# Optimization experiments

Hardware: AMD Instinct MI355X
Metric: run time of the kernel (lower is better)

## Reference

```python
import jax, jax.numpy as jnp
import numpy as np

VOCAB_SIZE = 128
HIDDEN_DIM = 128
NUM_STATES = 64
STACK_VOCAB_SIZE = 32
STACK_DEPTH = 64
NUM_MEM_ACTIONS = 2 + STACK_VOCAB_SIZE  # 0=NOOP, 1=POP, k>=2 => PUSH symbol (k-2)
NUM_BUF_ACTIONS = VOCAB_SIZE
T, B = 512, 512


def setup_inputs() -> dict:
    key = jax.random.key(0)
    ks = jax.random.split(key, 10)
    return {
        "x": jax.random.randint(ks[0], (T, B), 0, VOCAB_SIZE),
        "true_act": jax.random.randint(ks[1], (T, B), 0, NUM_MEM_ACTIONS),
        "true_s": jax.random.randint(ks[2], (T, B), 0, NUM_STATES),
        "use_forcing": jax.random.randint(ks[3], (T, B), 0, 2),
        "embed": jax.random.normal(ks[4], (VOCAB_SIZE, HIDDEN_DIM), jnp.float32) * 0.02,
        "W_mem": jax.random.normal(ks[5], (HIDDEN_DIM + NUM_STATES + STACK_VOCAB_SIZE, NUM_MEM_ACTIONS), jnp.float32) * 0.05,
        "b_mem": jnp.zeros((NUM_MEM_ACTIONS,), jnp.float32),
        "W_buf": jax.random.normal(ks[6], (HIDDEN_DIM + NUM_STATES + STACK_VOCAB_SIZE, NUM_BUF_ACTIONS), jnp.float32) * 0.05,
        "b_buf": jnp.zeros((NUM_BUF_ACTIONS,), jnp.float32),
        "W_state": jax.random.normal(ks[7], (HIDDEN_DIM + NUM_STATES + STACK_VOCAB_SIZE, NUM_STATES), jnp.float32) * 0.05,
        "b_state": jnp.zeros((NUM_STATES,), jnp.float32),
    }


def update_stack(stack, ptr, action):
    # stack: [STACK_DEPTH] int, ptr: [] int, action: [] int
    is_push = action >= 2
    is_pop = action == 1
    new_ptr = jnp.clip(ptr + jnp.where(is_push, 1, 0) - jnp.where(is_pop, 1, 0), 0, STACK_DEPTH - 1)
    sym = jnp.maximum(action - 2, 0)
    stack_new = stack.at[new_ptr].set(jnp.where(is_push, sym, stack[new_ptr]))
    r_new = stack_new[new_ptr]  # read top of stack
    return stack_new, new_ptr, r_new


def reference(x, true_act, true_s, use_forcing, embed, W_mem, b_mem, W_buf, b_buf, W_state, b_state):
    def step(carry, inp):
        stack, ptr, r_prev, s_prev = carry
        x_t, t_act, t_s, forcing = inp
        x_emb = embed[x_t]                                   # [B, H] gather
        s_emb = jax.nn.one_hot(s_prev, NUM_STATES, dtype=embed.dtype)
        r_emb = jax.nn.one_hot(r_prev, STACK_VOCAB_SIZE, dtype=embed.dtype)
        flat = jnp.concatenate([x_emb, s_emb, r_emb], axis=-1)  # [B, 224]
        logits_mem = flat @ W_mem + b_mem
        logits_buf = flat @ W_buf + b_buf
        logits_state = flat @ W_state + b_state
        pred_act = jnp.argmax(logits_mem, axis=-1)
        pred_state = jnp.argmax(logits_state, axis=-1)
        action = jnp.where(forcing > 0, t_act, pred_act)
        next_s = jnp.where(forcing > 0, t_s, pred_state)
        stack_new, ptr_new, r_new = jax.vmap(update_stack)(stack, ptr, action)
        return (stack_new, ptr_new, r_new, next_s), (logits_mem, logits_buf, logits_state)

    init = (
        jnp.zeros((B, STACK_DEPTH), jnp.int32),
        jnp.zeros((B,), jnp.int32),
        jnp.zeros((B,), jnp.int32),
        jnp.zeros((B,), jnp.int32),
    )
    _, (lm, lb, ls) = jax.lax.scan(step, init, (x, true_act, true_s, use_forcing))
    return lm, lb, ls
```

## Files before the change

### kernel.cpp

```cpp
#include <hip/hip_runtime.h>
#include <stdint.h>
#include <limits.h>


#define TT 512
#define BB 512
#define HH 128
#define NSs 64
#define NMm 34
#define NBb 128

typedef unsigned short u16;
typedef float f2 __attribute__((ext_vector_type(2)));

__global__ __launch_bounds__(256) void precompute_M(
    const float* __restrict__ embed,
    const float* __restrict__ Wm, const float* __restrict__ bm,
    const float* __restrict__ Wb, const float* __restrict__ bb,
    const float* __restrict__ Ws, const float* __restrict__ bs,
    float* __restrict__ Mm32, float* __restrict__ Ms32,
    float* __restrict__ Mb32, float* __restrict__ MmT,
    float* __restrict__ MsT) {
  __shared__ double e[HH];
  const int v = blockIdx.x;
  const int tid = threadIdx.x;
  if (tid < HH) e[tid] = (double)embed[v * HH + tid];
  __syncthreads();
  if (tid < NMm) {
    const int j = tid;
    double acc = 0.0;
    for (int h = 0; h < HH; ++h) acc += e[h] * (double)Wm[h * NMm + j];
    const float r = (float)(acc + (double)bm[j]);
    Mm32[v * NMm + j] = r;
    MmT[j * 128 + v] = r;
  } else if (tid < NMm + NSs) {
    const int j = tid - NMm;
    double acc = 0.0;
    for (int h = 0; h < HH; ++h) acc += e[h] * (double)Ws[h * NSs + j];
    const float r = (float)(acc + (double)bs[j]);
    Ms32[v * NSs + j] = r;
    MsT[j * 128 + v] = r;
  } else if (tid < NMm + NSs + NBb) {
    const int j = tid - NMm - NSs;
    double acc = 0.0;
    for (int h = 0; h < HH; ++h) acc += e[h] * (double)Wb[h * NBb + j];
    Mb32[v * NBb + j] = (float)(acc + (double)bb[j]);
  }
}

__global__ __launch_bounds__(128) void build_lut(
    const float* __restrict__ Wm, const float* __restrict__ Ws,
    const float* __restrict__ MmT, const float* __restrict__ MsT,
    u16* __restrict__ lut) {
  __shared__ float wms[NMm], wmr[NMm], wss[NSs], wsr[NSs];
  const int s = blockIdx.x >> 5;
  const int r = blockIdx.x & 31;
  const int tid = threadIdx.x;
  if (tid < NMm) {
    wms[tid] = Wm[(128 + s) * NMm + tid];
    wmr[tid] = Wm[(192 + r) * NMm + tid];
  }
  if (tid < NSs) {
    wss[tid] = Ws[(128 + s) * NSs + tid];
    wsr[tid] = Ws[(192 + r) * NSs + tid];
  }
  __syncthreads();

  const int v = tid;
  int bestm = INT_MIN, act = 0;
#pragma unroll
  for (int j = 0; j < NMm; ++j) {
    const double val = (double)MmT[j * 128 + v] + (double)wms[j] + (double)wmr[j];
    const int iv = (int)(val * 67108864.0);
    if (iv > bestm) { bestm = iv; act = j; }
  }
  int bests = INT_MIN, ns = 0;
#pragma unroll
  for (int j = 0; j < NSs; ++j) {
    const double val = (double)MsT[j * 128 + v] + (double)wss[j] + (double)wsr[j];
    const int iv = (int)(val * 67108864.0);
    if (iv > bests) { bests = iv; ns = j; }
  }
  lut[(unsigned)blockIdx.x * 128 + v] = (u16)(act | (ns << 6));
}

__global__ __launch_bounds__(512, 1) void sm_fused(
    const int* __restrict__ x, const int* __restrict__ tact,
    const int* __restrict__ tstate, const int* __restrict__ forc,
    const u16* __restrict__ lut,
    const float* __restrict__ Wm, const float* __restrict__ Wb,
    const float* __restrict__ Ws,
    const float* __restrict__ Mm32, const float* __restrict__ Ms32,
    const float* __restrict__ Mb32, float* __restrict__ out) {
  __shared__ unsigned sPk[2][TT];
  __shared__ volatile u16 trajL[2][TT];
  __shared__ volatile unsigned cnt[2];
  const int tid = threadIdx.x;
  const int base = blockIdx.x * 2;
  if (tid < 2) cnt[tid] = 0;
  for (int i = tid; i < 2 * TT; i += 512) {
    const int c = i >> 9, t = i & (TT - 1);
    const int g = t * BB + base + c;
    sPk[c][t] = (unsigned)x[g] | ((unsigned)tact[g] << 8) |
                ((unsigned)tstate[g] << 16) | ((unsigned)forc[g] << 24);
  }
  __syncthreads();

  const int lane = tid & 63;
  const int w = tid >> 6;

  if (w < 2) {
    __builtin_amdgcn_s_setprio(1);
    const int c = w;
    int stackv = 0;
    int ptr = 0, rr = 0, s = 0;
    unsigned p0 = sPk[c][0], p1 = sPk[c][1], p2 = sPk[c][2];

    for (int t = 0; t < TT; ++t) {
      const unsigned p3 = sPk[c][t + 3 < TT ? t + 3 : TT - 1];
      const unsigned pk_s = __builtin_amdgcn_readfirstlane(p0);

      if (lane == 0) trajL[c][t] = (u16)(s | (rr << 8));

      int act, ns;
      if (pk_s >> 24) {
        act = (int)((p0 >> 8) & 63u);
        ns = (int)((p0 >> 16) & 63u);
      } else {
        const int idx = s * 4096 + rr * 128 + (int)(p0 & 127u);
        const int lv = lut[idx];
        act = lv & 63;
        ns = (lv >> 6) & 63;
      }

      const bool ispush = act >= 2;
      int npn = ptr + (ispush ? 1 : 0) - (act == 1 ? 1 : 0);
      npn = npn < 0 ? 0 : (npn > 63 ? 63 : npn);
      if (ispush && lane == npn) stackv = act - 2;
      rr = __builtin_amdgcn_ds_bpermute(npn * 4, stackv);
      ptr = npn;
      s = ns;

      if ((t & 7) == 7) {
        __threadfence_block();
        if (lane == 0) cnt[c] = (unsigned)(t + 1);
      }
      p0 = p1; p1 = p2; p2 = p3;
    }
  } else {
    const int c = (w - 2) & 1;
    const int j = (w - 2) >> 1;
    const int b = base + c;
    float* outLM = out;
    float* outLB = out + (size_t)TT * BB * NMm;
    float* outLS = out + (size_t)TT * BB * (NMm + NBb);

    for (int t = j; t < TT; t += 3) {
      while (cnt[c] <= (unsigned)t) __builtin_amdgcn_s_sleep(4);
      const unsigned pk = sPk[c][t];
      const int xv = (int)(pk & 127u);
      const int pr = trajL[c][t];
      const int s = pr & 255;
      const int r = pr >> 8;
      const int rs = 128 + s, rr = 192 + r;
      const int row = t * BB + b;
      if (lane < NMm)
        __builtin_nontemporal_store(
            Mm32[xv * NMm + lane] + Wm[rs * NMm + lane] + Wm[rr * NMm + lane],
            &outLM[(size_t)row * NMm + lane]);
      __builtin_nontemporal_store(
          Ms32[xv * NSs + lane] + Ws[rs * NSs + lane] + Ws[rr * NSs + lane],
          &outLS[(size_t)row * NSs + lane]);
      const f2 mb  = *(const f2*)&Mb32[xv * NBb + 2 * lane];
      const f2 wbs = *(const f2*)&Wb[rs * NBb + 2 * lane];
      const f2 wbr = *(const f2*)&Wb[rr * NBb + 2 * lane];
      f2 o;
      o.x = mb.x + wbs.x + wbr.x;
      o.y = mb.y + wbs.y + wbr.y;
      __builtin_nontemporal_store(o, (f2*)&outLB[(size_t)row * NBb + 2 * lane]);
    }
  }
}

extern "C" void kernel_launch(void* const* d_in, const int* in_sizes, int n_in,
                              void* d_out, int out_size, void* d_ws, size_t ws_size,
                              hipStream_t stream) {
  if (ws_size < 690176) return;

  const int* x     = (const int*)d_in[0];
  const int* tactp = (const int*)d_in[1];
  const int* tstp  = (const int*)d_in[2];
  const int* forcp = (const int*)d_in[3];
  const float* embed = (const float*)d_in[4];
  const float* Wm = (const float*)d_in[5];
  const float* bm = (const float*)d_in[6];
  const float* Wb = (const float*)d_in[7];
  const float* bb = (const float*)d_in[8];
  const float* Ws = (const float*)d_in[9];
  const float* bs = (const float*)d_in[10];

  char* wsp = (char*)d_ws;
  float* Mm32 = (float*)(wsp);
  float* Ms32 = (float*)(wsp + 17408);
  float* Mb32 = (float*)(wsp + 50176);
  float* MmT  = (float*)(wsp + 115712);
  float* MsT  = (float*)(wsp + 133120);
  u16*   lut  = (u16*)(wsp + 165888);

  precompute_M<<<128, 256, 0, stream>>>(embed, Wm, bm, Wb, bb, Ws, bs,
                                        Mm32, Ms32, Mb32, MmT, MsT);
  build_lut<<<2048, 128, 0, stream>>>(Wm, Ws, MmT, MsT, lut);
  sm_fused<<<256, 512, 0, stream>>>(x, tactp, tstp, forcp, lut,
                                    Wm, Wb, Ws, Mm32, Ms32, Mb32,
                                    (float*)d_out);
}
```

Measured before the change: 156.0 us.

## Use one batch column per block with sentinel-based per-step producer/consumer sync

Each block now handles a single batch element instead of two: one wave runs the serial stack recurrence and seven waves write the logits. Blocks double to 512 so more CUs take part in the serial chain. The periodic shared counter with a fence every 8 steps is replaced by writing a sentinel into each trajectory slot and having consumers poll that slot. This lets consumers start each step as soon as it is ready, at the cost of more polling and relying on volatile ordering of 16-bit LDS stores without an explicit fence.

```diff
diff --git a/kernel.cpp b/kernel.cpp
--- a/kernel.cpp
+++ b/kernel.cpp
@@ -92,35 +92,32 @@
     const float* __restrict__ Ws,
     const float* __restrict__ Mm32, const float* __restrict__ Ms32,
     const float* __restrict__ Mb32, float* __restrict__ out) {
-  __shared__ unsigned sPk[2][TT];
-  __shared__ volatile u16 trajL[2][TT];
-  __shared__ volatile unsigned cnt[2];
+  __shared__ unsigned sPk[TT];
+  __shared__ volatile u16 trajL[TT];
   const int tid = threadIdx.x;
-  const int base = blockIdx.x * 2;
-  if (tid < 2) cnt[tid] = 0;
-  for (int i = tid; i < 2 * TT; i += 512) {
-    const int c = i >> 9, t = i & (TT - 1);
-    const int g = t * BB + base + c;
-    sPk[c][t] = (unsigned)x[g] | ((unsigned)tact[g] << 8) |
-                ((unsigned)tstate[g] << 16) | ((unsigned)forc[g] << 24);
+  const int b = blockIdx.x;
+  for (int t = tid; t < TT; t += 512) {
+    const int g = t * BB + b;
+    sPk[t] = (unsigned)x[g] | ((unsigned)tact[g] << 8) |
+             ((unsigned)tstate[g] << 16) | ((unsigned)forc[g] << 24);
+    trajL[t] = 0xFFFFu;
   }
   __syncthreads();
 
   const int lane = tid & 63;
   const int w = tid >> 6;
 
-  if (w < 2) {
+  if (w == 0) {
     __builtin_amdgcn_s_setprio(1);
-    const int c = w;
     int stackv = 0;
     int ptr = 0, rr = 0, s = 0;
-    unsigned p0 = sPk[c][0], p1 = sPk[c][1], p2 = sPk[c][2];
+    unsigned p0 = sPk[0], p1 = sPk[1], p2 = sPk[2];
 
     for (int t = 0; t < TT; ++t) {
-      const unsigned p3 = sPk[c][t + 3 < TT ? t + 3 : TT - 1];
+      const unsigned p3 = sPk[t + 3 < TT ? t + 3 : TT - 1];
       const unsigned pk_s = __builtin_amdgcn_readfirstlane(p0);
 
-      if (lane == 0) trajL[c][t] = (u16)(s | (rr << 8));
+      if (lane == 0) trajL[t] = (u16)(s | (rr << 8));
 
       int act, ns;
       if (pk_s >> 24) {
@@ -141,25 +138,22 @@
       ptr = npn;
       s = ns;
 
-      if ((t & 7) == 7) {
-        __threadfence_block();
-        if (lane == 0) cnt[c] = (unsigned)(t + 1);
-      }
       p0 = p1; p1 = p2; p2 = p3;
     }
   } else {
-    const int c = (w - 2) & 1;
-    const int j = (w - 2) >> 1;
-    const int b = base + c;
+    const int j = w - 1;
     float* outLM = out;
     float* outLB = out + (size_t)TT * BB * NMm;
     float* outLS = out + (size_t)TT * BB * (NMm + NBb);
 
-    for (int t = j; t < TT; t += 3) {
-      while (cnt[c] <= (unsigned)t) __builtin_amdgcn_s_sleep(4);
-      const unsigned pk = sPk[c][t];
+    for (int t = j; t < TT; t += 7) {
+      int pr = trajL[t];
+      while (pr == 0xFFFF) {
+        __builtin_amdgcn_s_sleep(4);
+        pr = trajL[t];
+      }
+      const unsigned pk = sPk[t];
       const int xv = (int)(pk & 127u);
-      const int pr = trajL[c][t];
       const int s = pr & 255;
       const int r = pr >> 8;
       const int rs = 128 + s, rr = 192 + r;
@@ -210,7 +204,7 @@
   precompute_M<<<128, 256, 0, stream>>>(embed, Wm, bm, Wb, bb, Ws, bs,
                                         Mm32, Ms32, Mb32, MmT, MsT);
   build_lut<<<2048, 128, 0, stream>>>(Wm, Ws, MmT, MsT, lut);
-  sm_fused<<<256, 512, 0, stream>>>(x, tactp, tstp, forcp, lut,
+  sm_fused<<<512, 512, 0, stream>>>(x, tactp, tstp, forcp, lut,
                                     Wm, Wb, Ws, Mm32, Ms32, Mb32,
                                     (float*)d_out);
 }
```

New measurement: 152.0 us. -2.6%, faster.
